# Performance work log

Measured on AMD Instinct MI355X. Metric: run time of the kernel, lower is better.

## Reference

```python
import math
import jax, jax.numpy as jnp
import numpy as np
from jax import lax

DN = ('NCHW', 'OIHW', 'NCHW')

def _blur(x):
    # upfirdn2d blur: separable [1,3,3,1] kernel, normalized, gain=factor^2=4, pad (1,1)
    k1 = jnp.asarray([1., 3., 3., 1.], dtype=x.dtype)
    k2 = jnp.outer(k1, k1)
    k2 = k2 / jnp.sum(k2) * 4.0
    C = x.shape[1]
    kern = jnp.broadcast_to(k2[None, None], (C, 1, 4, 4))
    return lax.conv_general_dilated(x, kern, (1, 1), [(1, 1), (1, 1)],
                                    feature_group_count=C, dimension_numbers=DN)

def _mod_conv(x, z, w, mw, mb, demodulate, upsample):
    # StyleGAN2 ModulatedConv2d. w: [Co,Ci,k,k]; mw: [Ci,style_dim]; mb: [Ci].
    # Equivalent formulation: scale input by style (per in-channel), conv with
    # base weight, rescale output by per-sample demod (per out-channel).
    Ci, k = w.shape[1], w.shape[-1]
    style = z @ mw.T * (1.0 / math.sqrt(mw.shape[1])) + mb  # EqualLinear -> [B, Ci]
    ws = w * (1.0 / math.sqrt(Ci * k * k))
    if demodulate:
        wmod = ws[None] * style[:, None, :, None, None]              # [B,Co,Ci,k,k]
        demod = lax.rsqrt(jnp.sum(wmod * wmod, axis=(2, 3, 4)) + 1e-8)  # [B,Co]
    x = x * style[:, :, None, None]
    if upsample:
        # torch conv_transpose2d(stride=2, pad=0) == direct conv with flipped kernel + lhs dilation
        kern = ws[:, :, ::-1, ::-1]
        x = lax.conv_general_dilated(x, kern, (1, 1), [(k - 1, k - 1)] * 2,
                                     lhs_dilation=(2, 2), dimension_numbers=DN)
    else:
        x = lax.conv_general_dilated(x, ws, (1, 1), [(k // 2, k // 2)] * 2,
                                     dimension_numbers=DN)
    if demodulate:
        x = x * demod[:, :, None, None]
    if upsample:
        x = _blur(x)
    return x

def _styled_conv(x, z, w, mw, mb, b, upsample):
    # StyledConv (use_noise=False): modulated conv + FusedLeakyReLU(bias, 0.2, gain sqrt(2))
    x = _mod_conv(x, z, w, mw, mb, True, upsample)
    return jax.nn.leaky_relu(x + b[None, :, None, None], 0.2) * math.sqrt(2.0)

def setup_inputs() -> dict:
    B, CIN, SD, S = 16, 256, 512, 32
    key = jax.random.key(0)
    ks = jax.random.split(key, 32)
    f32 = jnp.float32
    d = {
        'fg_feat': jax.random.normal(ks[0], (B, CIN, S, S), f32),
        'mask':    jax.random.uniform(ks[1], (B, S, S), f32),
        'bg_feat': jax.random.normal(ks[2], (B, CIN, S, S), f32),
        'z':       jax.random.normal(ks[3], (B, SD), f32),
    }
    # layer schedule: (cin, cout, upsample)
    layers = [(CIN, 128, False), (128, 128, True), (128, 64, False),
              (64, 64, True), (64, 32, False)]
    i = 4
    for li, (ci, co, _) in enumerate(layers):
        d[f'l{li}_w'] = jax.random.normal(ks[i], (co, ci, 3, 3), f32); i += 1
        d[f'l{li}_mw'] = jax.random.normal(ks[i], (ci, SD), f32); i += 1
        d[f'l{li}_mb'] = jnp.ones((ci,), f32)
        d[f'l{li}_b'] = jnp.zeros((co,), f32)
    d['fin_w'] = jax.random.normal(ks[i], (4, 32, 1, 1), f32); i += 1
    d['fin_mw'] = jax.random.normal(ks[i], (32, SD), f32); i += 1
    d['fin_mb'] = jnp.ones((32,), f32)
    d['out_bias'] = jnp.zeros((1, 4, 1, 1), f32)
    return d

def reference(fg_feat, mask, bg_feat, z,
              l0_w, l0_mw, l0_mb, l0_b,
              l1_w, l1_mw, l1_mb, l1_b,
              l2_w, l2_mw, l2_mb, l2_b,
              l3_w, l3_mw, l3_mb, l3_b,
              l4_w, l4_mw, l4_mb, l4_b,
              fin_w, fin_mw, fin_mb, out_bias):
    # bg_activation is None -> no bg transform
    h = fg_feat + (1.0 - mask[:, None]) * bg_feat          # [B,256,32,32]
    h = _styled_conv(h, z, l0_w, l0_mw, l0_mb, l0_b, False)  # [B,128,32,32]
    h = _styled_conv(h, z, l1_w, l1_mw, l1_mb, l1_b, True)   # [B,128,64,64]
    h = _styled_conv(h, z, l2_w, l2_mw, l2_mb, l2_b, False)  # [B,64,64,64]
    h = _styled_conv(h, z, l3_w, l3_mw, l3_mb, l3_b, True)   # [B,64,128,128]
    h = _styled_conv(h, z, l4_w, l4_mw, l4_mb, l4_b, False)  # [B,32,128,128]
    h = _mod_conv(h, z, fin_w, fin_mw, fin_mb, False, False) + out_bias  # [B,4,128,128]
    return h[:, :3]
```

## Files before the change

### kernel.cpp

```cpp
#include <hip/hip_runtime.h>
#include <math.h>

#define SQRT2 1.41421356237309515f

typedef __bf16 bf16x8 __attribute__((ext_vector_type(8)));
typedef float f32x4 __attribute__((ext_vector_type(4)));
typedef unsigned short u16x4 __attribute__((ext_vector_type(4)));
typedef unsigned short u16x8 __attribute__((ext_vector_type(8)));

__device__ __forceinline__ unsigned short f2bf(float f) {
    unsigned u = __builtin_bit_cast(unsigned, f);
    u += 0x7fffu + ((u >> 16) & 1u);
    return (unsigned short)(u >> 16);
}

__global__ __launch_bounds__(256) void style_all(
    const float* __restrict__ z,
    const float* __restrict__ mw0, const float* __restrict__ mb0,
    const float* __restrict__ mw1, const float* __restrict__ mb1,
    const float* __restrict__ mw2, const float* __restrict__ mb2,
    const float* __restrict__ mw3, const float* __restrict__ mb3,
    const float* __restrict__ mw4, const float* __restrict__ mb4,
    const float* __restrict__ mwf, const float* __restrict__ mbf,
    float* __restrict__ s0, float* __restrict__ s1, float* __restrict__ s2,
    float* __restrict__ s3, float* __restrict__ s4, float* __restrict__ sf) {
    int i = blockIdx.x * 256 + threadIdx.x;
    const float* mw; const float* mb; float* o; int Ci, idx; float mul = 1.f;
    if (i < 4096)       { mw = mw0; mb = mb0; o = s0; Ci = 256; idx = i; }
    else if (i < 6144)  { mw = mw1; mb = mb1; o = s1; Ci = 128; idx = i - 4096; }
    else if (i < 8192)  { mw = mw2; mb = mb2; o = s2; Ci = 128; idx = i - 6144; }
    else if (i < 9216)  { mw = mw3; mb = mb3; o = s3; Ci = 64;  idx = i - 8192; }
    else if (i < 10240) { mw = mw4; mb = mb4; o = s4; Ci = 64;  idx = i - 9216; }
    else if (i < 10752) { mw = mwf; mb = mbf; o = sf; Ci = 32;  idx = i - 10240;
                          mul = 0.1767766952966369f; }
    else return;
    int b = idx / Ci, ci = idx % Ci;
    const float* zp = z + b * 512;
    const float* wp = mw + ci * 512;
    float acc = 0.f;
#pragma unroll 8
    for (int k = 0; k < 512; ++k) acc += zp[k] * wp[k];
    o[idx] = (acc * 0.04419417382415922f + mb[ci]) * mul;
}

__global__ __launch_bounds__(256) void demod_all(
    const float* __restrict__ w0, const float* __restrict__ w1,
    const float* __restrict__ w2, const float* __restrict__ w3,
    const float* __restrict__ w4,
    const float* __restrict__ s0, const float* __restrict__ s1,
    const float* __restrict__ s2, const float* __restrict__ s3,
    const float* __restrict__ s4,
    float* __restrict__ d0, float* __restrict__ d1, float* __restrict__ d2,
    float* __restrict__ d3, float* __restrict__ d4) {
    int wid = blockIdx.x * 4 + (threadIdx.x >> 6);
    int lane = threadIdx.x & 63;
    const float* w; const float* s; float* d; int Co, Ci, idx;
    if (wid < 2048)      { w = w0; s = s0; d = d0; Co = 128; Ci = 256; idx = wid; }
    else if (wid < 4096) { w = w1; s = s1; d = d1; Co = 128; Ci = 128; idx = wid - 2048; }
    else if (wid < 5120) { w = w2; s = s2; d = d2; Co = 64;  Ci = 128; idx = wid - 4096; }
    else if (wid < 6144) { w = w3; s = s3; d = d3; Co = 64;  Ci = 64;  idx = wid - 5120; }
    else if (wid < 6656) { w = w4; s = s4; d = d4; Co = 32;  Ci = 64;  idx = wid - 6144; }
    else return;
    int b = idx / Co, co = idx % Co;
    const float* wp = w + (size_t)co * Ci * 9;
    const float* sp = s + b * Ci;
    float acc = 0.f;
    for (int k = lane; k < Ci * 9; k += 64) {
        int ci = k / 9;
        float v = wp[k], sv = sp[ci];
        acc += v * v * sv * sv;
    }
    for (int off = 32; off > 0; off >>= 1) acc += __shfl_down(acc, off);
    if (lane == 0) d[b * Co + co] = rsqrtf(acc / (float)(Ci * 9) + 1e-8f);
}

__device__ __forceinline__ void pack_cw_elem(
    const float* __restrict__ w, unsigned short* __restrict__ dst,
    int i, int Ci, int KT, float sInv) {
    int cil = i & 31;
    int r = i >> 5;
    int col = r % 32; r /= 32;
    int t = r % 9; r /= 9;
    int c = r % KT, g = r / KT;
    int co = g * 32 + col, ci = c * 32 + cil;
    dst[i] = f2bf(w[((size_t)co * Ci + ci) * 9 + t] * sInv);
}
__device__ __forceinline__ void pack_fused_elem(
    const float* __restrict__ w, unsigned short* __restrict__ dst,
    int i, int Ci, int KT, float sInv) {
    int cil = i & 31;
    int r = i >> 5;
    int col = r % 32; r /= 32;
    int t = r % 36; r /= 36;
    int c = r % KT, g = r / KT;
    int co = g * 32 + col, ci = c * 32 + cil;
    int p = t / 9, dd = (t % 9) / 3, ee = t % 3;
    int py = p >> 1, px = p & 1;
    const float k1[4] = {1.f, 3.f, 3.f, 1.f};
    const float* wq = w + ((size_t)co * Ci + ci) * 9;
    float acc = 0.f;
#pragma unroll
    for (int rr = 0; rr < 3; ++rr) {
        int ia = 2 * dd + rr - 1 - py;
        if (ia < 0 || ia > 3) continue;
#pragma unroll
        for (int ss = 0; ss < 3; ++ss) {
            int ib = 2 * ee + ss - 1 - px;
            if (ib < 0 || ib > 3) continue;
            acc += wq[rr * 3 + ss] * k1[ia] * k1[ib];
        }
    }
    dst[i] = f2bf(acc * sInv * (1.f / 16.f));
}

__global__ __launch_bounds__(256) void pack_all(
    const float* __restrict__ l0w, const float* __restrict__ l1w,
    const float* __restrict__ l2w, const float* __restrict__ l3w,
    const float* __restrict__ l4w, unsigned short* __restrict__ base) {
    const float sInv1152 = 0.02946278254943948f;
    int i = blockIdx.x * 256 + threadIdx.x;
    if (i < 294912)       pack_cw_elem(l0w, base, i, 256, 8, 1.f / 48.f);
    else if (i < 368640)  pack_cw_elem(l2w, base + 294912, i - 294912, 128, 4, sInv1152);
    else if (i < 387072)  pack_cw_elem(l4w, base + 368640, i - 368640, 64, 2, 1.f / 24.f);
    else if (i < 976896)  pack_fused_elem(l1w, base + 387072, i - 387072, 128, 4, sInv1152);
    else if (i < 1124352) pack_fused_elem(l3w, base + 976896, i - 976896, 64, 2, 1.f / 24.f);
}

__global__ __launch_bounds__(256) void composite_cl_kernel(
    const float* __restrict__ fg, const float* __restrict__ mask,
    const float* __restrict__ bg, const float* __restrict__ sty0,
    unsigned short* __restrict__ out) {
    __shared__ unsigned short ldsT[32 * 264];
    int blk = blockIdx.x;
    int b = blk >> 5, y = blk & 31;
    int t = threadIdx.x;
    int x = t & 31, cr = t >> 5;
    const float* sb = sty0 + b * 256;
    float m = 1.f - mask[(b << 10) + (y << 5) + x];
    for (int k = 0; k < 32; ++k) {
        int ci = k * 8 + cr;
        size_t idx = ((size_t)(b * 256 + ci) << 10) + (y << 5) + x;
        float v = fg[idx] + m * bg[idx];
        ldsT[x * 264 + ci] = f2bf(v * sb[ci]);
    }
    __syncthreads();
    int xx = t >> 5, cu = t & 31;
#pragma unroll
    for (int ph = 0; ph < 4; ++ph) {
        int px = ph * 8 + xx;
        u16x8 v = *(const u16x8*)&ldsT[px * 264 + cu * 8];
        *(u16x8*)(out + (((size_t)(b * 32 + y) * 32 + px) << 8) + cu * 8) = v;
    }
}

template <int OUTMODE>
__global__ __launch_bounds__(256, 4) void conv3x3_cl(
    const unsigned short* __restrict__ X, const unsigned short* __restrict__ W,
    const float* __restrict__ demod, const float* __restrict__ bias,
    const float* __restrict__ nextsty, const float* __restrict__ finw,
    const float* __restrict__ ob, void* __restrict__ outv,
    int Ci, int Co, int S, int TPS, int KCH, int cogN) {
    __shared__ unsigned short ldsX[324 * 40];
    const int tid = threadIdx.x;
    const int b = blockIdx.z;
    const int gy_ = blockIdx.y;
    const int ks = gy_ / cogN, cog = gy_ % cogN;
    const int tile = blockIdx.x;
    const int ty0 = (tile / TPS) * 16, tx0 = (tile % TPS) * 16;
    const int KT = Ci >> 5;
    const int wave = tid >> 6, lane = tid & 63, quad = lane >> 4, l16 = lane & 15;

    f32x4 acc[2][4];
#pragma unroll
    for (int mt = 0; mt < 2; ++mt)
#pragma unroll
        for (int nt = 0; nt < 4; ++nt) acc[mt][nt] = (f32x4){0.f, 0.f, 0.f, 0.f};

    for (int cc = 0; cc < KCH; ++cc) {
        const int cg = ks * KCH + cc;
        const int ci0 = cg * 32;
        for (int u = tid; u < 1296; u += 256) {
            int sp = u >> 2, cq = u & 3;
            int y = sp / 18, xx = sp - y * 18;
            int gy = ty0 - 1 + y, gx = tx0 - 1 + xx;
            u16x8 pk = (u16x8){0, 0, 0, 0, 0, 0, 0, 0};
            if ((unsigned)gy < (unsigned)S && (unsigned)gx < (unsigned)S)
                pk = *(const u16x8*)(X + ((size_t)(b * S + gy) * S + gx) * Ci + ci0 + cq * 8);
            *(u16x8*)&ldsX[sp * 40 + cq * 8] = pk;
        }
        __syncthreads();
        const unsigned short* wt = W + (((size_t)cog * KT + cg) * 9) * 1024;
#pragma unroll
        for (int t = 0; t < 9; ++t) {
            const int ty = t / 3, tx = t - ty * 3;
            bf16x8 af[2];
#pragma unroll
            for (int mt = 0; mt < 2; ++mt)
                af[mt] = *(const bf16x8*)(const void*)(wt + t * 1024 + (mt * 16 + l16) * 32 + quad * 8);
#pragma unroll
            for (int nt = 0; nt < 4; ++nt) {
                int sp = (wave * 4 + nt + ty) * 18 + l16 + tx;
                bf16x8 bv = *(const bf16x8*)(const void*)&ldsX[sp * 40 + quad * 8];
#pragma unroll
                for (int mt = 0; mt < 2; ++mt)
                    acc[mt][nt] = __builtin_amdgcn_mfma_f32_16x16x32_bf16(af[mt], bv, acc[mt][nt], 0, 0, 0);
            }
        }
        __syncthreads();
    }
    const int col = tx0 + l16;
    if (OUTMODE == 0) {
        float* out = (float*)outv;
        const size_t PS = (size_t)16 * S * S * Co;
#pragma unroll
        for (int mt = 0; mt < 2; ++mt) {
            int co0 = cog * 32 + mt * 16 + quad * 4;
#pragma unroll
            for (int nt = 0; nt < 4; ++nt) {
                int row = ty0 + wave * 4 + nt;
                *(f32x4*)&out[ks * PS + ((size_t)(b * S + row) * S + col) * Co + co0] = acc[mt][nt];
            }
        }
    } else if (OUTMODE == 1) {
#pragma unroll
        for (int mt = 0; mt < 2; ++mt) {
            int co0 = cog * 32 + mt * 16 + quad * 4;
            f32x4 dm = *(const f32x4*)&demod[b * Co + co0];
            f32x4 bi = *(const f32x4*)&bias[co0];
            f32x4 ns = *(const f32x4*)&nextsty[b * Co + co0];
#pragma unroll
            for (int nt = 0; nt < 4; ++nt) {
                int row = ty0 + wave * 4 + nt;
                size_t base = ((size_t)(b * S + row) * S + col) * Co + co0;
                u16x4 st;
#pragma unroll
                for (int r = 0; r < 4; ++r) {
                    float v = acc[mt][nt][r] * dm[r] + bi[r];
                    v = (v > 0.f ? v : 0.2f * v) * SQRT2 * ns[r];
                    st[r] = f2bf(v);
                }
                *(u16x4*)((unsigned short*)outv + base) = st;
            }
        }
    } else {
        f32x4 dm[2], bi[2], ns[2];
        float fw[3][2][4];
#pragma unroll
        for (int mt = 0; mt < 2; ++mt) {
            int c0 = mt * 16 + quad * 4;
            dm[mt] = *(const f32x4*)&demod[b * Co + c0];
            bi[mt] = *(const f32x4*)&bias[c0];
            ns[mt] = *(const f32x4*)&nextsty[b * Co + c0];
#pragma unroll
            for (int c = 0; c < 3; ++c)
#pragma unroll
                for (int r = 0; r < 4; ++r) fw[c][mt][r] = finw[c * 32 + c0 + r];
        }
        float* out = (float*)outv;
        float ob0 = ob[0], ob1 = ob[1], ob2 = ob[2];
#pragma unroll
        for (int nt = 0; nt < 4; ++nt) {
            int row = ty0 + wave * 4 + nt;
            float p0 = 0.f, p1 = 0.f, p2 = 0.f;
#pragma unroll
            for (int mt = 0; mt < 2; ++mt)
#pragma unroll
                for (int r = 0; r < 4; ++r) {
                    float v = acc[mt][nt][r] * dm[mt][r] + bi[mt][r];
                    v = (v > 0.f ? v : 0.2f * v) * SQRT2 * ns[mt][r];
                    p0 += v * fw[0][mt][r];
                    p1 += v * fw[1][mt][r];
                    p2 += v * fw[2][mt][r];
                }
            p0 += __shfl_xor(p0, 16); p0 += __shfl_xor(p0, 32);
            p1 += __shfl_xor(p1, 16); p1 += __shfl_xor(p1, 32);
            p2 += __shfl_xor(p2, 16); p2 += __shfl_xor(p2, 32);
            if (quad == 0) {
                size_t base = (((size_t)b * 3) << 14) + (row << 7) + col;
                out[base] = p0 + ob0;
                out[base + 16384] = p1 + ob1;
                out[base + 32768] = p2 + ob2;
            }
        }
    }
}

__global__ __launch_bounds__(256) void combine_l0_kernel(
    const float* __restrict__ P, const float* __restrict__ demod,
    const float* __restrict__ bias, const float* __restrict__ sty1,
    unsigned short* __restrict__ out) {
    int i = blockIdx.x * 256 + threadIdx.x;
    int co = i & 127;
    int b = i >> 17;
    float v = P[i] + P[i + (1 << 21)];
    v = v * demod[b * 128 + co] + bias[co];
    v = (v > 0.f ? v : 0.2f * v) * SQRT2 * sty1[b * 128 + co];
    out[i] = f2bf(v);
}

__global__ __launch_bounds__(256, 4) void upblur_cl(
    const unsigned short* __restrict__ X, const unsigned short* __restrict__ EW,
    const float* __restrict__ demod, const float* __restrict__ bias,
    const float* __restrict__ nextsty, unsigned short* __restrict__ out,
    int Ci, int Co, int S, int TPS) {
    __shared__ unsigned short ldsX[324 * 40];
    const int tid = threadIdx.x;
    const int b = blockIdx.z;
    const int cog = blockIdx.y >> 2, p = blockIdx.y & 3;
    const int tile = blockIdx.x;
    const int ty0 = (tile / TPS) * 16, tx0 = (tile % TPS) * 16;
    const int KT = Ci >> 5;
    const int wave = tid >> 6, lane = tid & 63, quad = lane >> 4, l16 = lane & 15;

    f32x4 acc[2][4];
#pragma unroll
    for (int mt = 0; mt < 2; ++mt)
#pragma unroll
        for (int nt = 0; nt < 4; ++nt) acc[mt][nt] = (f32x4){0.f, 0.f, 0.f, 0.f};

    for (int cc = 0; cc < KT; ++cc) {
        const int ci0 = cc * 32;
        for (int u = tid; u < 1296; u += 256) {
            int sp = u >> 2, cq = u & 3;
            int y = sp / 18, xx = sp - y * 18;
            int gy = ty0 - 1 + y, gx = tx0 - 1 + xx;
            u16x8 pk = (u16x8){0, 0, 0, 0, 0, 0, 0, 0};
            if ((unsigned)gy < (unsigned)S && (unsigned)gx < (unsigned)S)
                pk = *(const u16x8*)(X + ((size_t)(b * S + gy) * S + gx) * Ci + ci0 + cq * 8);
            *(u16x8*)&ldsX[sp * 40 + cq * 8] = pk;
        }
        __syncthreads();
        const unsigned short* wt = EW + (((size_t)cog * KT + cc) * 36 + p * 9) * 1024;
#pragma unroll
        for (int t = 0; t < 9; ++t) {
            const int dd = t / 3, ee = t - dd * 3;
            bf16x8 af[2];
#pragma unroll
            for (int mt = 0; mt < 2; ++mt)
                af[mt] = *(const bf16x8*)(const void*)(wt + t * 1024 + (mt * 16 + l16) * 32 + quad * 8);
#pragma unroll
            for (int nt = 0; nt < 4; ++nt) {
                int sp = (wave * 4 + nt + dd) * 18 + l16 + ee;
                bf16x8 bv = *(const bf16x8*)(const void*)&ldsX[sp * 40 + quad * 8];
#pragma unroll
                for (int mt = 0; mt < 2; ++mt)
                    acc[mt][nt] = __builtin_amdgcn_mfma_f32_16x16x32_bf16(af[mt], bv, acc[mt][nt], 0, 0, 0);
            }
        }
        __syncthreads();
    }
    const int S2 = 2 * S;
    const int py = p >> 1, px = p & 1;
    const int Xc = tx0 + l16, ox = 2 * Xc + px;
#pragma unroll
    for (int mt = 0; mt < 2; ++mt) {
        const int co0 = cog * 32 + mt * 16 + quad * 4;
        f32x4 dm = *(const f32x4*)&demod[b * Co + co0];
        f32x4 bi = *(const f32x4*)&bias[co0];
        f32x4 ns = *(const f32x4*)&nextsty[b * Co + co0];
#pragma unroll
        for (int nt = 0; nt < 4; ++nt) {
            int Y = ty0 + wave * 4 + nt, oy = 2 * Y + py;
            u16x4 st;
#pragma unroll
            for (int r = 0; r < 4; ++r) {
                float v = acc[mt][nt][r] * dm[r] + bi[r];
                v = (v > 0.f ? v : 0.2f * v) * SQRT2 * ns[r];
                st[r] = f2bf(v);
            }
            *(u16x4*)(out + ((size_t)(b * S2 + oy) * S2 + ox) * Co + co0) = st;
        }
    }
}

extern "C" void kernel_launch(void* const* d_in, const int* in_sizes, int n_in,
                              void* d_out, int out_size, void* d_ws, size_t ws_size,
                              hipStream_t stream) {
    const float* fg   = (const float*)d_in[0];
    const float* mask = (const float*)d_in[1];
    const float* bg   = (const float*)d_in[2];
    const float* z    = (const float*)d_in[3];
    const float* l0_w = (const float*)d_in[4];
    const float* l0_mw= (const float*)d_in[5];
    const float* l0_mb= (const float*)d_in[6];
    const float* l0_b = (const float*)d_in[7];
    const float* l1_w = (const float*)d_in[8];
    const float* l1_mw= (const float*)d_in[9];
    const float* l1_mb= (const float*)d_in[10];
    const float* l1_b = (const float*)d_in[11];
    const float* l2_w = (const float*)d_in[12];
    const float* l2_mw= (const float*)d_in[13];
    const float* l2_mb= (const float*)d_in[14];
    const float* l2_b = (const float*)d_in[15];
    const float* l3_w = (const float*)d_in[16];
    const float* l3_mw= (const float*)d_in[17];
    const float* l3_mb= (const float*)d_in[18];
    const float* l3_b = (const float*)d_in[19];
    const float* l4_w = (const float*)d_in[20];
    const float* l4_mw= (const float*)d_in[21];
    const float* l4_mb= (const float*)d_in[22];
    const float* l4_b = (const float*)d_in[23];
    const float* fin_w = (const float*)d_in[24];
    const float* fin_mw= (const float*)d_in[25];
    const float* fin_mb= (const float*)d_in[26];
    const float* obias = (const float*)d_in[27];

    float* wsf = (float*)d_ws;
    float* sty0 = wsf + 0;
    float* sty1 = wsf + 4096;
    float* sty2 = wsf + 6144;
    float* sty3 = wsf + 8192;
    float* sty4 = wsf + 9216;
    float* styf = wsf + 10240;
    float* dm0  = wsf + 10752;
    float* dm1  = wsf + 12800;
    float* dm2  = wsf + 14848;
    float* dm3  = wsf + 15872;
    float* dm4  = wsf + 16896;
    unsigned short* wbase = (unsigned short*)(wsf + 17408);
    unsigned short* wp0 = wbase;
    unsigned short* wp2 = wbase + 294912;
    unsigned short* wp4 = wbase + 368640;
    unsigned short* ew1 = wbase + 387072;
    unsigned short* ew3 = wbase + 976896;
    unsigned short* X0  = (unsigned short*)(wsf + 600000);
    float* Pbuf = wsf + 2697152;
    unsigned short* Y0  = (unsigned short*)(wsf + 6891456);
    unsigned short* Z1  = (unsigned short*)(wsf + 7940032);
    unsigned short* Y2  = X0;
    unsigned short* Z3  = (unsigned short*)(wsf + 12134336);

    dim3 blk(256);

    style_all<<<42, blk, 0, stream>>>(z, l0_mw, l0_mb, l1_mw, l1_mb, l2_mw, l2_mb,
                                      l3_mw, l3_mb, l4_mw, l4_mb, fin_mw, fin_mb,
                                      sty0, sty1, sty2, sty3, sty4, styf);
    demod_all<<<1664, blk, 0, stream>>>(l0_w, l1_w, l2_w, l3_w, l4_w,
                                        sty0, sty1, sty2, sty3, sty4,
                                        dm0, dm1, dm2, dm3, dm4);
    pack_all<<<4392, blk, 0, stream>>>(l0_w, l1_w, l2_w, l3_w, l4_w, wbase);

    composite_cl_kernel<<<512, blk, 0, stream>>>(fg, mask, bg, sty0, X0);

    conv3x3_cl<0><<<dim3(4, 8, 16), blk, 0, stream>>>(X0, wp0, nullptr, nullptr, nullptr, nullptr, nullptr, Pbuf, 256, 128, 32, 2, 4, 4);
    combine_l0_kernel<<<8192, blk, 0, stream>>>(Pbuf, dm0, l0_b, sty1, Y0);

    upblur_cl<<<dim3(4, 16, 16), blk, 0, stream>>>(Y0, ew1, dm1, l1_b, sty2, Z1, 128, 128, 32, 2);

    conv3x3_cl<1><<<dim3(16, 2, 16), blk, 0, stream>>>(Z1, wp2, dm2, l2_b, sty3, nullptr, nullptr, Y2, 128, 64, 64, 4, 4, 2);

    upblur_cl<<<dim3(16, 8, 16), blk, 0, stream>>>(Y2, ew3, dm3, l3_b, sty4, Z3, 64, 64, 64, 4);

    conv3x3_cl<3><<<dim3(64, 1, 16), blk, 0, stream>>>(Z3, wp4, dm4, l4_b, styf, fin_w, obias, (float*)d_out, 64, 32, 128, 8, 2, 1);
}
```

Before: 305.1 us.

## Widen conv output-channel tiles, fuse upsample phases, register-prefetch input staging, split demod

The 3x3 conv kernels now compute up to 64 output channels per block (MT=4), and the upsample kernel computes all four transposed-conv phases in one block. Each LDS-staged input tile is therefore reused across more MFMAs, and the input is loaded once instead of once per phase or channel group. Input tiles are prefetched into registers for the next channel chunk while the current one is computed. Demodulation is split into a weight-square precompute plus a cheap per-sample reduction. In exchange, register pressure rises (launch bounds drop to 2 blocks per SM) and grids shrink, which may leave the GPU underfilled.

```diff
diff --git a/kernel.cpp b/kernel.cpp
--- a/kernel.cpp
+++ b/kernel.cpp
@@ -43,10 +43,27 @@
     o[idx] = (acc * 0.04419417382415922f + mb[ci]) * mul;
 }
 
-__global__ __launch_bounds__(256) void demod_all(
+__global__ __launch_bounds__(256) void wsq_all(
     const float* __restrict__ w0, const float* __restrict__ w1,
     const float* __restrict__ w2, const float* __restrict__ w3,
-    const float* __restrict__ w4,
+    const float* __restrict__ w4, float* __restrict__ q) {
+    int i = blockIdx.x * 256 + threadIdx.x;
+    const float* w; float* o; int idx;
+    if (i < 32768)      { w = w0; o = q;          idx = i; }
+    else if (i < 49152) { w = w1; o = q + 32768;  idx = i - 32768; }
+    else if (i < 57344) { w = w2; o = q + 49152;  idx = i - 49152; }
+    else if (i < 61440) { w = w3; o = q + 57344;  idx = i - 57344; }
+    else if (i < 63488) { w = w4; o = q + 61440;  idx = i - 61440; }
+    else return;
+    const float* wp = w + (size_t)idx * 9;
+    float a = 0.f;
+#pragma unroll
+    for (int t = 0; t < 9; ++t) a += wp[t] * wp[t];
+    o[idx] = a;
+}
+
+__global__ __launch_bounds__(256) void demod2_all(
+    const float* __restrict__ q,
     const float* __restrict__ s0, const float* __restrict__ s1,
     const float* __restrict__ s2, const float* __restrict__ s3,
     const float* __restrict__ s4,
@@ -54,21 +71,20 @@
     float* __restrict__ d3, float* __restrict__ d4) {
     int wid = blockIdx.x * 4 + (threadIdx.x >> 6);
     int lane = threadIdx.x & 63;
-    const float* w; const float* s; float* d; int Co, Ci, idx;
-    if (wid < 2048)      { w = w0; s = s0; d = d0; Co = 128; Ci = 256; idx = wid; }
-    else if (wid < 4096) { w = w1; s = s1; d = d1; Co = 128; Ci = 128; idx = wid - 2048; }
-    else if (wid < 5120) { w = w2; s = s2; d = d2; Co = 64;  Ci = 128; idx = wid - 4096; }
-    else if (wid < 6144) { w = w3; s = s3; d = d3; Co = 64;  Ci = 64;  idx = wid - 5120; }
-    else if (wid < 6656) { w = w4; s = s4; d = d4; Co = 32;  Ci = 64;  idx = wid - 6144; }
+    const float* qp; const float* s; float* d; int Co, Ci, idx;
+    if (wid < 2048)      { qp = q;         s = s0; d = d0; Co = 128; Ci = 256; idx = wid; }
+    else if (wid < 4096) { qp = q + 32768; s = s1; d = d1; Co = 128; Ci = 128; idx = wid - 2048; }
+    else if (wid < 5120) { qp = q + 49152; s = s2; d = d2; Co = 64;  Ci = 128; idx = wid - 4096; }
+    else if (wid < 6144) { qp = q + 57344; s = s3; d = d3; Co = 64;  Ci = 64;  idx = wid - 5120; }
+    else if (wid < 6656) { qp = q + 61440; s = s4; d = d4; Co = 32;  Ci = 64;  idx = wid - 6144; }
     else return;
     int b = idx / Co, co = idx % Co;
-    const float* wp = w + (size_t)co * Ci * 9;
+    const float* wp = qp + (size_t)co * Ci;
     const float* sp = s + b * Ci;
     float acc = 0.f;
-    for (int k = lane; k < Ci * 9; k += 64) {
-        int ci = k / 9;
-        float v = wp[k], sv = sp[ci];
-        acc += v * v * sv * sv;
+    for (int k = lane; k < Ci; k += 64) {
+        float sv = sp[k];
+        acc += wp[k] * sv * sv;
     }
     for (int off = 32; off > 0; off >>= 1) acc += __shfl_down(acc, off);
     if (lane == 0) d[b * Co + co] = rsqrtf(acc / (float)(Ci * 9) + 1e-8f);
@@ -153,8 +169,39 @@
     }
 }
 
-template <int OUTMODE>
-__global__ __launch_bounds__(256, 4) void conv3x3_cl(
+__device__ __forceinline__ void stage_issue(
+    u16x8 pk[6], const unsigned short* __restrict__ X,
+    int b, int S, int Ci, int ci0, int ty0, int tx0, int tid) {
+#pragma unroll
+    for (int j = 0; j < 6; ++j) {
+        int u = tid + j * 256;
+        bool ok = (j < 5) || (tid < 16);
+        int sp = u >> 2, cq = u & 3;
+        int y = sp / 18, xx = sp - y * 18;
+        int gy = ty0 - 1 + y, gx = tx0 - 1 + xx;
+        u16x8 v = (u16x8){0, 0, 0, 0, 0, 0, 0, 0};
+        if (ok && (unsigned)gy < (unsigned)S && (unsigned)gx < (unsigned)S)
+            v = *(const u16x8*)(X + ((size_t)(b * S + gy) * S + gx) * Ci + ci0 + cq * 8);
+        pk[j] = v;
+    }
+}
+__device__ __forceinline__ void stage_write(
+    const u16x8 pk[6], unsigned short* ldsX, int tid) {
+#pragma unroll
+    for (int j = 0; j < 5; ++j) {
+        int u = tid + j * 256;
+        int sp = u >> 2, cq = u & 3;
+        *(u16x8*)&ldsX[sp * 40 + cq * 8] = pk[j];
+    }
+    if (tid < 16) {
+        int u = tid + 1280;
+        int sp = u >> 2, cq = u & 3;
+        *(u16x8*)&ldsX[sp * 40 + cq * 8] = pk[5];
+    }
+}
+
+template <int OUTMODE, int MT>
+__global__ __launch_bounds__(256, 2) void conv3x3_cl(
     const unsigned short* __restrict__ X, const unsigned short* __restrict__ W,
     const float* __restrict__ demod, const float* __restrict__ bias,
     const float* __restrict__ nextsty, const float* __restrict__ finw,
@@ -170,40 +217,37 @@
     const int KT = Ci >> 5;
     const int wave = tid >> 6, lane = tid & 63, quad = lane >> 4, l16 = lane & 15;
 
-    f32x4 acc[2][4];
-#pragma unroll
-    for (int mt = 0; mt < 2; ++mt)
+    f32x4 acc[MT][4];
+#pragma unroll
+    for (int mt = 0; mt < MT; ++mt)
 #pragma unroll
         for (int nt = 0; nt < 4; ++nt) acc[mt][nt] = (f32x4){0.f, 0.f, 0.f, 0.f};
 
+    u16x8 pk[6];
+    stage_issue(pk, X, b, S, Ci, (ks * KCH) * 32, ty0, tx0, tid);
     for (int cc = 0; cc < KCH; ++cc) {
         const int cg = ks * KCH + cc;
-        const int ci0 = cg * 32;
-        for (int u = tid; u < 1296; u += 256) {
-            int sp = u >> 2, cq = u & 3;
-            int y = sp / 18, xx = sp - y * 18;
-            int gy = ty0 - 1 + y, gx = tx0 - 1 + xx;
-            u16x8 pk = (u16x8){0, 0, 0, 0, 0, 0, 0, 0};
-            if ((unsigned)gy < (unsigned)S && (unsigned)gx < (unsigned)S)
-                pk = *(const u16x8*)(X + ((size_t)(b * S + gy) * S + gx) * Ci + ci0 + cq * 8);
-            *(u16x8*)&ldsX[sp * 40 + cq * 8] = pk;
-        }
+        stage_write(pk, ldsX, tid);
         __syncthreads();
-        const unsigned short* wt = W + (((size_t)cog * KT + cg) * 9) * 1024;
+        if (cc + 1 < KCH)
+            stage_issue(pk, X, b, S, Ci, (cg + 1) * 32, ty0, tx0, tid);
 #pragma unroll
         for (int t = 0; t < 9; ++t) {
             const int ty = t / 3, tx = t - ty * 3;
-            bf16x8 af[2];
-#pragma unroll
-            for (int mt = 0; mt < 2; ++mt)
-                af[mt] = *(const bf16x8*)(const void*)(wt + t * 1024 + (mt * 16 + l16) * 32 + quad * 8);
+            bf16x8 bv[4];
 #pragma unroll
             for (int nt = 0; nt < 4; ++nt) {
                 int sp = (wave * 4 + nt + ty) * 18 + l16 + tx;
-                bf16x8 bv = *(const bf16x8*)(const void*)&ldsX[sp * 40 + quad * 8];
-#pragma unroll
-                for (int mt = 0; mt < 2; ++mt)
-                    acc[mt][nt] = __builtin_amdgcn_mfma_f32_16x16x32_bf16(af[mt], bv, acc[mt][nt], 0, 0, 0);
+                bv[nt] = *(const bf16x8*)(const void*)&ldsX[sp * 40 + quad * 8];
+            }
+#pragma unroll
+            for (int mt = 0; mt < MT; ++mt) {
+                const unsigned short* wt =
+                    W + (((size_t)(cog * (MT / 2) + (mt >> 1)) * KT + cg) * 9 + t) * 1024;
+                bf16x8 af = *(const bf16x8*)(const void*)(wt + ((mt & 1) * 16 + l16) * 32 + quad * 8);
+#pragma unroll
+                for (int nt = 0; nt < 4; ++nt)
+                    acc[mt][nt] = __builtin_amdgcn_mfma_f32_16x16x32_bf16(af, bv[nt], acc[mt][nt], 0, 0, 0);
             }
         }
         __syncthreads();
@@ -213,8 +257,8 @@
         float* out = (float*)outv;
         const size_t PS = (size_t)16 * S * S * Co;
 #pragma unroll
-        for (int mt = 0; mt < 2; ++mt) {
-            int co0 = cog * 32 + mt * 16 + quad * 4;
+        for (int mt = 0; mt < MT; ++mt) {
+            int co0 = cog * (MT * 16) + mt * 16 + quad * 4;
 #pragma unroll
             for (int nt = 0; nt < 4; ++nt) {
                 int row = ty0 + wave * 4 + nt;
@@ -223,8 +267,8 @@
         }
     } else if (OUTMODE == 1) {
 #pragma unroll
-        for (int mt = 0; mt < 2; ++mt) {
-            int co0 = cog * 32 + mt * 16 + quad * 4;
+        for (int mt = 0; mt < MT; ++mt) {
+            int co0 = cog * (MT * 16) + mt * 16 + quad * 4;
             f32x4 dm = *(const f32x4*)&demod[b * Co + co0];
             f32x4 bi = *(const f32x4*)&bias[co0];
             f32x4 ns = *(const f32x4*)&nextsty[b * Co + co0];
@@ -243,10 +287,10 @@
             }
         }
     } else {
-        f32x4 dm[2], bi[2], ns[2];
-        float fw[3][2][4];
-#pragma unroll
-        for (int mt = 0; mt < 2; ++mt) {
+        f32x4 dm[MT], bi[MT], ns[MT];
+        float fw[3][MT][4];
+#pragma unroll
+        for (int mt = 0; mt < MT; ++mt) {
             int c0 = mt * 16 + quad * 4;
             dm[mt] = *(const f32x4*)&demod[b * Co + c0];
             bi[mt] = *(const f32x4*)&bias[c0];
@@ -263,7 +307,7 @@
             int row = ty0 + wave * 4 + nt;
             float p0 = 0.f, p1 = 0.f, p2 = 0.f;
 #pragma unroll
-            for (int mt = 0; mt < 2; ++mt)
+            for (int mt = 0; mt < MT; ++mt)
 #pragma unroll
                 for (int r = 0; r < 4; ++r) {
                     float v = acc[mt][nt][r] * dm[mt][r] + bi[mt][r];
@@ -298,7 +342,7 @@
     out[i] = f2bf(v);
 }
 
-__global__ __launch_bounds__(256, 4) void upblur_cl(
+__global__ __launch_bounds__(256, 2) void upblur_cl(
     const unsigned short* __restrict__ X, const unsigned short* __restrict__ EW,
     const float* __restrict__ demod, const float* __restrict__ bias,
     const float* __restrict__ nextsty, unsigned short* __restrict__ out,
@@ -306,52 +350,53 @@
     __shared__ unsigned short ldsX[324 * 40];
     const int tid = threadIdx.x;
     const int b = blockIdx.z;
-    const int cog = blockIdx.y >> 2, p = blockIdx.y & 3;
+    const int cog = blockIdx.y;
     const int tile = blockIdx.x;
     const int ty0 = (tile / TPS) * 16, tx0 = (tile % TPS) * 16;
     const int KT = Ci >> 5;
     const int wave = tid >> 6, lane = tid & 63, quad = lane >> 4, l16 = lane & 15;
 
-    f32x4 acc[2][4];
-#pragma unroll
-    for (int mt = 0; mt < 2; ++mt)
-#pragma unroll
-        for (int nt = 0; nt < 4; ++nt) acc[mt][nt] = (f32x4){0.f, 0.f, 0.f, 0.f};
-
+    f32x4 acc[4][2][4];
+#pragma unroll
+    for (int p = 0; p < 4; ++p)
+#pragma unroll
+        for (int mt = 0; mt < 2; ++mt)
+#pragma unroll
+            for (int nt = 0; nt < 4; ++nt) acc[p][mt][nt] = (f32x4){0.f, 0.f, 0.f, 0.f};
+
+    u16x8 pk[6];
+    stage_issue(pk, X, b, S, Ci, 0, ty0, tx0, tid);
     for (int cc = 0; cc < KT; ++cc) {
-        const int ci0 = cc * 32;
-        for (int u = tid; u < 1296; u += 256) {
-            int sp = u >> 2, cq = u & 3;
-            int y = sp / 18, xx = sp - y * 18;
-            int gy = ty0 - 1 + y, gx = tx0 - 1 + xx;
-            u16x8 pk = (u16x8){0, 0, 0, 0, 0, 0, 0, 0};
-            if ((unsigned)gy < (unsigned)S && (unsigned)gx < (unsigned)S)
-                pk = *(const u16x8*)(X + ((size_t)(b * S + gy) * S + gx) * Ci + ci0 + cq * 8);
-            *(u16x8*)&ldsX[sp * 40 + cq * 8] = pk;
-        }
+        stage_write(pk, ldsX, tid);
         __syncthreads();
-        const unsigned short* wt = EW + (((size_t)cog * KT + cc) * 36 + p * 9) * 1024;
+        if (cc + 1 < KT)
+            stage_issue(pk, X, b, S, Ci, (cc + 1) * 32, ty0, tx0, tid);
+        const unsigned short* wt0 = EW + (((size_t)cog * KT + cc) * 36) * 1024;
 #pragma unroll
         for (int t = 0; t < 9; ++t) {
             const int dd = t / 3, ee = t - dd * 3;
-            bf16x8 af[2];
-#pragma unroll
-            for (int mt = 0; mt < 2; ++mt)
-                af[mt] = *(const bf16x8*)(const void*)(wt + t * 1024 + (mt * 16 + l16) * 32 + quad * 8);
+            bf16x8 bv[4];
 #pragma unroll
             for (int nt = 0; nt < 4; ++nt) {
                 int sp = (wave * 4 + nt + dd) * 18 + l16 + ee;
-                bf16x8 bv = *(const bf16x8*)(const void*)&ldsX[sp * 40 + quad * 8];
-#pragma unroll
-                for (int mt = 0; mt < 2; ++mt)
-                    acc[mt][nt] = __builtin_amdgcn_mfma_f32_16x16x32_bf16(af[mt], bv, acc[mt][nt], 0, 0, 0);
+                bv[nt] = *(const bf16x8*)(const void*)&ldsX[sp * 40 + quad * 8];
+            }
+#pragma unroll
+            for (int p = 0; p < 4; ++p) {
+                const unsigned short* wt = wt0 + ((size_t)(p * 9 + t)) * 1024;
+                bf16x8 af0 = *(const bf16x8*)(const void*)(wt + l16 * 32 + quad * 8);
+                bf16x8 af1 = *(const bf16x8*)(const void*)(wt + (16 + l16) * 32 + quad * 8);
+#pragma unroll
+                for (int nt = 0; nt < 4; ++nt) {
+                    acc[p][0][nt] = __builtin_amdgcn_mfma_f32_16x16x32_bf16(af0, bv[nt], acc[p][0][nt], 0, 0, 0);
+                    acc[p][1][nt] = __builtin_amdgcn_mfma_f32_16x16x32_bf16(af1, bv[nt], acc[p][1][nt], 0, 0, 0);
+                }
             }
         }
         __syncthreads();
     }
     const int S2 = 2 * S;
-    const int py = p >> 1, px = p & 1;
-    const int Xc = tx0 + l16, ox = 2 * Xc + px;
+    const int Xc = tx0 + l16;
 #pragma unroll
     for (int mt = 0; mt < 2; ++mt) {
         const int co0 = cog * 32 + mt * 16 + quad * 4;
@@ -359,16 +404,21 @@
         f32x4 bi = *(const f32x4*)&bias[co0];
         f32x4 ns = *(const f32x4*)&nextsty[b * Co + co0];
 #pragma unroll
-        for (int nt = 0; nt < 4; ++nt) {
-            int Y = ty0 + wave * 4 + nt, oy = 2 * Y + py;
-            u16x4 st;
-#pragma unroll
-            for (int r = 0; r < 4; ++r) {
-                float v = acc[mt][nt][r] * dm[r] + bi[r];
-                v = (v > 0.f ? v : 0.2f * v) * SQRT2 * ns[r];
-                st[r] = f2bf(v);
-            }
-            *(u16x4*)(out + ((size_t)(b * S2 + oy) * S2 + ox) * Co + co0) = st;
+        for (int p = 0; p < 4; ++p) {
+            const int py = p >> 1, px = p & 1;
+            const int ox = 2 * Xc + px;
+#pragma unroll
+            for (int nt = 0; nt < 4; ++nt) {
+                int Y = ty0 + wave * 4 + nt, oy = 2 * Y + py;
+                u16x4 st;
+#pragma unroll
+                for (int r = 0; r < 4; ++r) {
+                    float v = acc[p][mt][nt][r] * dm[r] + bi[r];
+                    v = (v > 0.f ? v : 0.2f * v) * SQRT2 * ns[r];
+                    st[r] = f2bf(v);
+                }
+                *(u16x4*)(out + ((size_t)(b * S2 + oy) * S2 + ox) * Co + co0) = st;
+            }
         }
     }
 }
@@ -429,27 +479,28 @@
     unsigned short* Z1  = (unsigned short*)(wsf + 7940032);
     unsigned short* Y2  = X0;
     unsigned short* Z3  = (unsigned short*)(wsf + 12134336);
+    float* wsq = Pbuf;
 
     dim3 blk(256);
 
     style_all<<<42, blk, 0, stream>>>(z, l0_mw, l0_mb, l1_mw, l1_mb, l2_mw, l2_mb,
                                       l3_mw, l3_mb, l4_mw, l4_mb, fin_mw, fin_mb,
                                       sty0, sty1, sty2, sty3, sty4, styf);
-    demod_all<<<1664, blk, 0, stream>>>(l0_w, l1_w, l2_w, l3_w, l4_w,
-                                        sty0, sty1, sty2, sty3, sty4,
-                                        dm0, dm1, dm2, dm3, dm4);
+    wsq_all<<<248, blk, 0, stream>>>(l0_w, l1_w, l2_w, l3_w, l4_w, wsq);
+    demod2_all<<<1664, blk, 0, stream>>>(wsq, sty0, sty1, sty2, sty3, sty4,
+                                         dm0, dm1, dm2, dm3, dm4);
     pack_all<<<4392, blk, 0, stream>>>(l0_w, l1_w, l2_w, l3_w, l4_w, wbase);
 
     composite_cl_kernel<<<512, blk, 0, stream>>>(fg, mask, bg, sty0, X0);
 
-    conv3x3_cl<0><<<dim3(4, 8, 16), blk, 0, stream>>>(X0, wp0, nullptr, nullptr, nullptr, nullptr, nullptr, Pbuf, 256, 128, 32, 2, 4, 4);
+    conv3x3_cl<0, 4><<<dim3(4, 4, 16), blk, 0, stream>>>(X0, wp0, nullptr, nullptr, nullptr, nullptr, nullptr, Pbuf, 256, 128, 32, 2, 4, 2);
     combine_l0_kernel<<<8192, blk, 0, stream>>>(Pbuf, dm0, l0_b, sty1, Y0);
 
-    upblur_cl<<<dim3(4, 16, 16), blk, 0, stream>>>(Y0, ew1, dm1, l1_b, sty2, Z1, 128, 128, 32, 2);
-
-    conv3x3_cl<1><<<dim3(16, 2, 16), blk, 0, stream>>>(Z1, wp2, dm2, l2_b, sty3, nullptr, nullptr, Y2, 128, 64, 64, 4, 4, 2);
-
-    upblur_cl<<<dim3(16, 8, 16), blk, 0, stream>>>(Y2, ew3, dm3, l3_b, sty4, Z3, 64, 64, 64, 4);
-
-    conv3x3_cl<3><<<dim3(64, 1, 16), blk, 0, stream>>>(Z3, wp4, dm4, l4_b, styf, fin_w, obias, (float*)d_out, 64, 32, 128, 8, 2, 1);
-}
+    upblur_cl<<<dim3(4, 4, 16), blk, 0, stream>>>(Y0, ew1, dm1, l1_b, sty2, Z1, 128, 128, 32, 2);
+
+    conv3x3_cl<1, 4><<<dim3(16, 1, 16), blk, 0, stream>>>(Z1, wp2, dm2, l2_b, sty3, nullptr, nullptr, Y2, 128, 64, 64, 4, 4, 1);
+
+    upblur_cl<<<dim3(16, 2, 16), blk, 0, stream>>>(Y2, ew3, dm3, l3_b, sty4, Z3, 64, 64, 64, 4);
+
+    conv3x3_cl<3, 2><<<dim3(64, 1, 16), blk, 0, stream>>>(Z3, wp4, dm4, l4_b, styf, fin_w, obias, (float*)d_out, 64, 32, 128, 8, 2, 1);
+}
```

Result: slower. 400.0 us (+31.1%).
